# Kernel tuning notes

Measured on AMD Instinct MI355X. Metric: run time of the kernel, lower is better.

Reference implementation:

```python
import jax, jax.numpy as jnp
import numpy as np

N_NODES = 100000
N_EDGES = 1600000
N_FEAT = 32
HIDDEN = 96
N_GRAPHS = 2048


def setup_inputs() -> dict:
    key = jax.random.key(0)
    ks = jax.random.split(key, 16)
    x = jax.random.normal(ks[0], (N_NODES, N_FEAT), dtype=jnp.float32)
    edge_index = jax.random.randint(ks[1], (2, N_EDGES), 0, N_NODES, dtype=jnp.int64)
    batch = jnp.sort(jax.random.randint(ks[2], (N_NODES,), 0, N_GRAPHS, dtype=jnp.int64))

    def glorot(k, shape):
        lim = np.sqrt(6.0 / (shape[0] + shape[1]))
        return jax.random.uniform(k, shape, dtype=jnp.float32, minval=-lim, maxval=lim)

    return {
        "x": x, "edge_index": edge_index, "batch": batch,
        "W1": glorot(ks[3], (N_FEAT, HIDDEN)), "b1": jnp.zeros((HIDDEN,), jnp.float32),
        "W2": glorot(ks[4], (HIDDEN, HIDDEN)), "b2": jnp.zeros((HIDDEN,), jnp.float32),
        "W3": glorot(ks[5], (HIDDEN, HIDDEN)), "b3": jnp.zeros((HIDDEN,), jnp.float32),
        "W4": glorot(ks[6], (HIDDEN, HIDDEN)), "b4": jnp.zeros((HIDDEN,), jnp.float32),
        "Wf1": glorot(ks[7], (HIDDEN, 32)), "bf1": jnp.zeros((32,), jnp.float32),
        "Wf2": glorot(ks[8], (32, 1)), "bf2": jnp.zeros((1,), jnp.float32),
    }


def _gcn_norm(edge_index, num_nodes):
    # PyG GCNConv default: add self-loops, symmetric normalization D^-1/2 (A+I) D^-1/2
    loops = jnp.arange(num_nodes, dtype=edge_index.dtype)
    src = jnp.concatenate([edge_index[0], loops])
    dst = jnp.concatenate([edge_index[1], loops])
    deg = jax.ops.segment_sum(jnp.ones_like(dst, dtype=jnp.float32), dst, num_segments=num_nodes)
    dinv = jnp.where(deg > 0, jax.lax.rsqrt(jnp.where(deg > 0, deg, 1.0)), 0.0)
    norm = dinv[src] * dinv[dst]  # [E + N]
    return src, dst, norm


def _gcn_conv(x, src, dst, norm, W, b, num_nodes):
    xw = x @ W                      # [N, out]
    msg = xw[src] * norm[:, None]   # [E+N, out] gather + scale
    out = jax.ops.segment_sum(msg, dst, num_segments=num_nodes)  # scatter-add
    return out + b


def reference(x, edge_index, batch, W1, b1, W2, b2, W3, b3, W4, b4, Wf1, bf1, Wf2, bf2):
    n = x.shape[0]
    src, dst, norm = _gcn_norm(edge_index, n)
    h = jax.nn.relu(_gcn_conv(x, src, dst, norm, W1, b1, n))
    h = jax.nn.relu(_gcn_conv(h, src, dst, norm, W2, b2, n))
    h = jax.nn.relu(_gcn_conv(h, src, dst, norm, W3, b3, n))
    h = jax.nn.relu(_gcn_conv(h, src, dst, norm, W4, b4, n))
    g = jax.ops.segment_sum(h, batch, num_segments=N_GRAPHS)  # global_add_pool [G, 96]
    g = jax.nn.relu(g @ Wf1 + bf1)
    return g @ Wf2 + bf2  # [G, 1]
```

## Files before the change

kernel.cpp:

```cpp
#include <hip/hip_runtime.h>
#include <hip/hip_fp16.h>


#define HIDDEN 96

__device__ inline float4 h4_to_f4(uint2 u) {
    __half2 a = *reinterpret_cast<__half2*>(&u.x);
    __half2 b = *reinterpret_cast<__half2*>(&u.y);
    float2 fa = __half22float2(a), fb = __half22float2(b);
    return make_float4(fa.x, fa.y, fb.x, fb.y);
}

__device__ inline uint2 f4_to_h4(float4 v) {
    __half2 a = __float22half2_rn(make_float2(v.x, v.y));
    __half2 b = __float22half2_rn(make_float2(v.z, v.w));
    uint2 u;
    u.x = *reinterpret_cast<unsigned*>(&a);
    u.y = *reinterpret_cast<unsigned*>(&b);
    return u;
}

__global__ __launch_bounds__(256) void zero_int_kernel(int* p, int n) {
    int i = blockIdx.x * 256 + threadIdx.x;
    if (i < n) p[i] = 0;
}

__global__ __launch_bounds__(256) void zero_kernel(float* p, int n) {
    int i = blockIdx.x * 256 + threadIdx.x;
    if (i < n) p[i] = 0.0f;
}

__global__ __launch_bounds__(256) void cast_h_kernel(const float4* __restrict__ in,
                                                     uint2* __restrict__ out, int n4) {
    int i = blockIdx.x * 256 + threadIdx.x;
    if (i < n4) out[i] = f4_to_h4(in[i]);
}

__global__ __launch_bounds__(256) void deg_pos_kernel(const int* __restrict__ dst,
                                                      int* __restrict__ cnt,
                                                      int* __restrict__ epos, int E) {
    int e = blockIdx.x * 256 + threadIdx.x;
    if (e < E) epos[e] = atomicAdd(&cnt[dst[e]], 1);
}

__global__ __launch_bounds__(256) void dinv_kernel(const int* __restrict__ cnt,
                                                   float* __restrict__ dinv, int n) {
    int i = blockIdx.x * 256 + threadIdx.x;
    if (i < n) dinv[i] = rsqrtf((float)(cnt[i] + 1));
}

__global__ __launch_bounds__(256) void scan_reduce_kernel(const int* __restrict__ cnt,
                                                          int* __restrict__ bsum, int N) {
    __shared__ int s[256];
    int b = blockIdx.x, tid = threadIdx.x;
    int base = b * 1024;
    int v = 0;
    for (int j = tid; j < 1024; j += 256) {
        int i = base + j;
        v += (i < N) ? cnt[i] : 0;
    }
    s[tid] = v;
    __syncthreads();
    for (int off = 128; off > 0; off >>= 1) {
        if (tid < off) s[tid] += s[tid + off];
        __syncthreads();
    }
    if (tid == 0) bsum[b] = s[0];
}

__global__ __launch_bounds__(128) void scan_bsum_kernel(int* __restrict__ bsum, int nb) {
    __shared__ int s[128];
    int tid = threadIdx.x;
    int v = (tid < nb) ? bsum[tid] : 0;
    s[tid] = v;
    __syncthreads();
    for (int off = 1; off < 128; off <<= 1) {
        int t = (tid >= off) ? s[tid - off] : 0;
        __syncthreads();
        s[tid] += t;
        __syncthreads();
    }
    if (tid < nb) bsum[tid] = s[tid] - v;
}

__global__ __launch_bounds__(256) void scan_write_kernel(const int* __restrict__ cnt,
                                                         const int* __restrict__ bsum,
                                                         int* __restrict__ rowptr,
                                                         int N, int E) {
    __shared__ int ts[256];
    int b = blockIdx.x, tid = threadIdx.x;
    int base = b * 1024 + tid * 4;
    int v0 = (base + 0 < N) ? cnt[base + 0] : 0;
    int v1 = (base + 1 < N) ? cnt[base + 1] : 0;
    int v2 = (base + 2 < N) ? cnt[base + 2] : 0;
    int v3 = (base + 3 < N) ? cnt[base + 3] : 0;
    int sum = v0 + v1 + v2 + v3;
    ts[tid] = sum;
    __syncthreads();
    for (int off = 1; off < 256; off <<= 1) {
        int t = (tid >= off) ? ts[tid - off] : 0;
        __syncthreads();
        ts[tid] += t;
        __syncthreads();
    }
    int excl = bsum[b] + ts[tid] - sum;
    if (base + 0 < N) rowptr[base + 0] = excl;
    if (base + 1 < N) rowptr[base + 1] = excl + v0;
    if (base + 2 < N) rowptr[base + 2] = excl + v0 + v1;
    if (base + 3 < N) rowptr[base + 3] = excl + v0 + v1 + v2;
    if (b == 0 && tid == 0) rowptr[N] = E;
}

__global__ __launch_bounds__(256) void fill_csr_kernel(const int* __restrict__ src,
                                                       const int* __restrict__ dst,
                                                       const int* __restrict__ epos,
                                                       const float* __restrict__ dinv,
                                                       const int* __restrict__ rowptr,
                                                       int* __restrict__ col,
                                                       float* __restrict__ val, int E) {
    int e = blockIdx.x * 256 + threadIdx.x;
    if (e >= E) return;
    int s = src[e];
    int d = dst[e];
    int idx = rowptr[d] + epos[e];
    col[idx] = s;
    val[idx] = dinv[s] * dinv[d];
}

template <int K, bool RELU, bool BIAS, bool HALF_OUT>
__global__ __launch_bounds__(256) void gemm_kernel(const float* __restrict__ X,
                                                   const float* __restrict__ W,
                                                   const float* __restrict__ b,
                                                   void* __restrict__ Y, int n) {
    __shared__ float wlds[K * HIDDEN];
    for (int idx = threadIdx.x; idx < K * HIDDEN; idx += 256) wlds[idx] = W[idx];
    __syncthreads();

    int row = blockIdx.x * 256 + threadIdx.x;
    if (row >= n) return;

    float4 acc[24];
#pragma unroll
    for (int j = 0; j < 24; j++) acc[j] = make_float4(0.f, 0.f, 0.f, 0.f);

    const float4* wl4 = reinterpret_cast<const float4*>(wlds);
    const float4* xrow = reinterpret_cast<const float4*>(X + (size_t)row * K);

    for (int k0 = 0; k0 < K; k0 += 4) {
        float4 xv = xrow[k0 >> 2];
        if (RELU) {
            xv.x = fmaxf(xv.x, 0.f); xv.y = fmaxf(xv.y, 0.f);
            xv.z = fmaxf(xv.z, 0.f); xv.w = fmaxf(xv.w, 0.f);
        }
#pragma unroll
        for (int kk = 0; kk < 4; kk++) {
            float xs = (kk == 0) ? xv.x : (kk == 1) ? xv.y : (kk == 2) ? xv.z : xv.w;
#pragma unroll
            for (int j = 0; j < 24; j++) {
                float4 w = wl4[(k0 + kk) * 24 + j];
                acc[j].x += xs * w.x;
                acc[j].y += xs * w.y;
                acc[j].z += xs * w.z;
                acc[j].w += xs * w.w;
            }
        }
    }

#pragma unroll
    for (int j = 0; j < 24; j++) {
        if (BIAS) {
            float4 bb = reinterpret_cast<const float4*>(b)[j];
            acc[j].x += bb.x; acc[j].y += bb.y; acc[j].z += bb.z; acc[j].w += bb.w;
        }
    }
    if (HALF_OUT) {
        uint2* y2 = reinterpret_cast<uint2*>(Y) + (size_t)row * 24;
#pragma unroll
        for (int j = 0; j < 24; j++) y2[j] = f4_to_h4(acc[j]);
    } else {
        float4* y4 = reinterpret_cast<float4*>(Y) + (size_t)row * 24;
#pragma unroll
        for (int j = 0; j < 24; j++) y4[j] = acc[j];
    }
}

template <int TPN, bool POOL, bool BIAS>
__global__ __launch_bounds__(256) void aggregate_kernel(const uint2* __restrict__ xwh,
                                                        const int* __restrict__ rowptr,
                                                        const int* __restrict__ col,
                                                        const float* __restrict__ val,
                                                        const float* __restrict__ dinv,
                                                        const float* __restrict__ b,
                                                        float* __restrict__ out,
                                                        const int* __restrict__ batch,
                                                        float* __restrict__ gpool, int n) {
    unsigned t = blockIdx.x * 256 + threadIdx.x;
    unsigned i = t / (unsigned)TPN, q = t % (unsigned)TPN;
    if (i >= (unsigned)n) return;

    float dv = dinv[i];
    float s = dv * dv;
    float4 self = h4_to_f4(xwh[i * TPN + q]);
    float4 acc = make_float4(s * self.x, s * self.y, s * self.z, s * self.w);
    if (BIAS) {
        float4 bb = reinterpret_cast<const float4*>(b)[q];
        acc.x += bb.x; acc.y += bb.y; acc.z += bb.z; acc.w += bb.w;
    }

    int e = rowptr[i], end = rowptr[i + 1];
    for (; e + 3 < end; e += 4) {
        int c0 = col[e], c1 = col[e + 1], c2 = col[e + 2], c3 = col[e + 3];
        float w0 = val[e], w1 = val[e + 1], w2 = val[e + 2], w3 = val[e + 3];
        uint2 u0 = xwh[(unsigned)c0 * TPN + q];
        uint2 u1 = xwh[(unsigned)c1 * TPN + q];
        uint2 u2 = xwh[(unsigned)c2 * TPN + q];
        uint2 u3 = xwh[(unsigned)c3 * TPN + q];
        float4 v0 = h4_to_f4(u0), v1 = h4_to_f4(u1);
        float4 v2 = h4_to_f4(u2), v3 = h4_to_f4(u3);
        acc.x += w0 * v0.x + w1 * v1.x + w2 * v2.x + w3 * v3.x;
        acc.y += w0 * v0.y + w1 * v1.y + w2 * v2.y + w3 * v3.y;
        acc.z += w0 * v0.z + w1 * v1.z + w2 * v2.z + w3 * v3.z;
        acc.w += w0 * v0.w + w1 * v1.w + w2 * v2.w + w3 * v3.w;
    }
    for (; e < end; e++) {
        int c0 = col[e];
        float w0 = val[e];
        float4 g = h4_to_f4(xwh[(unsigned)c0 * TPN + q]);
        acc.x += w0 * g.x; acc.y += w0 * g.y;
        acc.z += w0 * g.z; acc.w += w0 * g.w;
    }

    if (POOL) {
        float* o = gpool + (size_t)batch[i] * (TPN * 4);
        unsigned fo = q * 4u;
        atomicAdd(o + fo + 0, fmaxf(acc.x, 0.f));
        atomicAdd(o + fo + 1, fmaxf(acc.y, 0.f));
        atomicAdd(o + fo + 2, fmaxf(acc.z, 0.f));
        atomicAdd(o + fo + 3, fmaxf(acc.w, 0.f));
    } else {
        reinterpret_cast<float4*>(out)[i * TPN + q] = acc;
    }
}

__global__ __launch_bounds__(64) void mlp_kernel(const float* __restrict__ g,
                                                 const float* __restrict__ Wf1,
                                                 const float* __restrict__ bf1,
                                                 const float* __restrict__ Wf2,
                                                 const float* __restrict__ bf2,
                                                 float* __restrict__ out, int G) {
    __shared__ float gs[HIDDEN];
    __shared__ float hid[32];
    int blk = blockIdx.x;
    int lane = threadIdx.x;
    for (int idx = lane; idx < HIDDEN; idx += 64) gs[idx] = g[(size_t)blk * HIDDEN + idx];
    __syncthreads();
    if (lane < 32) {
        float a = bf1[lane];
        for (int k = 0; k < HIDDEN; k++) a = fmaf(gs[k], Wf1[k * 32 + lane], a);
        hid[lane] = fmaxf(a, 0.f);
    }
    __syncthreads();
    if (lane == 0) {
        float o = bf2[0];
        for (int k = 0; k < 32; k++) o = fmaf(hid[k], Wf2[k], o);
        out[blk] = o;
    }
}

extern "C" void kernel_launch(void* const* d_in, const int* in_sizes, int n_in,
                              void* d_out, int out_size, void* d_ws, size_t ws_size,
                              hipStream_t stream) {
    const float* x     = (const float*)d_in[0];
    const int*   ei    = (const int*)d_in[1];
    const int*   batch = (const int*)d_in[2];
    const float* W1 = (const float*)d_in[3];  const float* b1 = (const float*)d_in[4];
    const float* W2 = (const float*)d_in[5];  const float* b2 = (const float*)d_in[6];
    const float* W3 = (const float*)d_in[7];  const float* b3 = (const float*)d_in[8];
    const float* W4 = (const float*)d_in[9];  const float* b4 = (const float*)d_in[10];
    const float* Wf1 = (const float*)d_in[11]; const float* bf1 = (const float*)d_in[12];
    const float* Wf2 = (const float*)d_in[13]; const float* bf2 = (const float*)d_in[14];
    float* out = (float*)d_out;

    int N = in_sizes[0] / 32;
    int E = in_sizes[1] / 2;
    int G = out_size;
    const int* src = ei;
    const int* dst = ei + E;

    char* ws = (char*)d_ws;
    size_t off = 0;
    auto alloc = [&](size_t bytes) -> void* {
        void* p = (void*)(ws + off);
        off += (bytes + 255) & ~(size_t)255;
        return p;
    };
    int*   degcnt = (int*)alloc((size_t)N * 4);
    float* dinv   = (float*)alloc((size_t)N * 4);
    int*   rowptr = (int*)alloc((size_t)(N + 1) * 4);
    int*   bsum   = (int*)alloc((size_t)128 * 4);
    int*   col    = (int*)alloc((size_t)E * 4);
    float* val    = (float*)alloc((size_t)E * 4);
    float* bufA   = (float*)alloc((size_t)N * 32 * 4);
    float* bufB   = (float*)alloc((size_t)N * HIDDEN * 4);
    uint2* bufH   = (uint2*)alloc((size_t)N * HIDDEN * 2);
    uint2* xh     = (uint2*)alloc((size_t)N * 32 * 2);
    float* gbuf   = (float*)alloc((size_t)G * HIDDEN * 4);
    (void)ws_size;

    int* epos = (int*)bufA;
    float* aggX = bufA;

    int gN   = (N + 255) / 256;
    int gE   = (E + 255) / 256;
    int gAgg32 = (int)(((long long)N * 8 + 255) / 256);
    int gAgg96 = (int)(((long long)N * 24 + 255) / 256);
    int nb   = (N + 1023) / 1024;

    zero_int_kernel<<<gN, 256, 0, stream>>>(degcnt, N);
    deg_pos_kernel<<<gE, 256, 0, stream>>>(dst, degcnt, epos, E);
    dinv_kernel<<<gN, 256, 0, stream>>>(degcnt, dinv, N);
    scan_reduce_kernel<<<nb, 256, 0, stream>>>(degcnt, bsum, N);
    scan_bsum_kernel<<<1, 128, 0, stream>>>(bsum, nb);
    scan_write_kernel<<<nb, 256, 0, stream>>>(degcnt, bsum, rowptr, N, E);
    fill_csr_kernel<<<gE, 256, 0, stream>>>(src, dst, epos, dinv, rowptr, col, val, E);

    cast_h_kernel<<<(N * 8 + 255) / 256, 256, 0, stream>>>(
        reinterpret_cast<const float4*>(x), xh, N * 8);
    aggregate_kernel<8, false, false><<<gAgg32, 256, 0, stream>>>(
        xh, rowptr, col, val, dinv, nullptr, aggX, nullptr, nullptr, N);
    gemm_kernel<32, false, true, false><<<gN, 256, 0, stream>>>(aggX, W1, b1, bufB, N);

    gemm_kernel<96, true, false, true><<<gN, 256, 0, stream>>>(bufB, W2, nullptr, bufH, N);
    aggregate_kernel<24, false, true><<<gAgg96, 256, 0, stream>>>(
        bufH, rowptr, col, val, dinv, b2, bufB, nullptr, nullptr, N);

    gemm_kernel<96, true, false, true><<<gN, 256, 0, stream>>>(bufB, W3, nullptr, bufH, N);
    aggregate_kernel<24, false, true><<<gAgg96, 256, 0, stream>>>(
        bufH, rowptr, col, val, dinv, b3, bufB, nullptr, nullptr, N);

    zero_kernel<<<(G * HIDDEN + 255) / 256, 256, 0, stream>>>(gbuf, G * HIDDEN);
    gemm_kernel<96, true, false, true><<<gN, 256, 0, stream>>>(bufB, W4, nullptr, bufH, N);
    aggregate_kernel<24, true, true><<<gAgg96, 256, 0, stream>>>(
        bufH, rowptr, col, val, dinv, b4, nullptr, batch, gbuf, N);

    mlp_kernel<<<G, 64, 0, stream>>>(gbuf, Wf1, bf1, Wf2, bf2, out, G);
}
```

Before: 704.8 us.

## Pad CSR rows to multiples of eight and store intermediates in fp16

Each CSR row is padded to a multiple of 8 entries, with zero col and val in the padding, so the aggregation loop issues vectorized int4/float4 loads of col and val and 8 gathers per iteration with no remainder loop. All intermediate activations (aggregation outputs and first GEMM output) are now stored in half precision, which halves the traffic of the GEMM and aggregate intermediates. In exchange there is extra zeroing of the padded col/val arrays, wasted gathers of row 0 for padding slots, and lower precision in the intermediate activations.

```diff
diff --git a/kernel.cpp b/kernel.cpp
--- a/kernel.cpp
+++ b/kernel.cpp
@@ -19,6 +19,8 @@
     u.y = *reinterpret_cast<unsigned*>(&b);
     return u;
 }
+
+__device__ inline int pad8(int c) { return (c + 7) & ~7; }
 
 __global__ __launch_bounds__(256) void zero_int_kernel(int* p, int n) {
     int i = blockIdx.x * 256 + threadIdx.x;
@@ -57,7 +59,7 @@
     int v = 0;
     for (int j = tid; j < 1024; j += 256) {
         int i = base + j;
-        v += (i < N) ? cnt[i] : 0;
+        v += (i < N) ? pad8(cnt[i]) : 0;
     }
     s[tid] = v;
     __syncthreads();
@@ -85,15 +87,14 @@
 
 __global__ __launch_bounds__(256) void scan_write_kernel(const int* __restrict__ cnt,
                                                          const int* __restrict__ bsum,
-                                                         int* __restrict__ rowptr,
-                                                         int N, int E) {
+                                                         int* __restrict__ rowptr, int N) {
     __shared__ int ts[256];
     int b = blockIdx.x, tid = threadIdx.x;
     int base = b * 1024 + tid * 4;
-    int v0 = (base + 0 < N) ? cnt[base + 0] : 0;
-    int v1 = (base + 1 < N) ? cnt[base + 1] : 0;
-    int v2 = (base + 2 < N) ? cnt[base + 2] : 0;
-    int v3 = (base + 3 < N) ? cnt[base + 3] : 0;
+    int v0 = (base + 0 < N) ? pad8(cnt[base + 0]) : 0;
+    int v1 = (base + 1 < N) ? pad8(cnt[base + 1]) : 0;
+    int v2 = (base + 2 < N) ? pad8(cnt[base + 2]) : 0;
+    int v3 = (base + 3 < N) ? pad8(cnt[base + 3]) : 0;
     int sum = v0 + v1 + v2 + v3;
     ts[tid] = sum;
     __syncthreads();
@@ -104,11 +105,10 @@
         __syncthreads();
     }
     int excl = bsum[b] + ts[tid] - sum;
-    if (base + 0 < N) rowptr[base + 0] = excl;
-    if (base + 1 < N) rowptr[base + 1] = excl + v0;
-    if (base + 2 < N) rowptr[base + 2] = excl + v0 + v1;
-    if (base + 3 < N) rowptr[base + 3] = excl + v0 + v1 + v2;
-    if (b == 0 && tid == 0) rowptr[N] = E;
+    if (base + 0 <= N) rowptr[base + 0] = excl;
+    if (base + 1 <= N) rowptr[base + 1] = excl + v0;
+    if (base + 2 <= N) rowptr[base + 2] = excl + v0 + v1;
+    if (base + 3 <= N) rowptr[base + 3] = excl + v0 + v1 + v2;
 }
 
 __global__ __launch_bounds__(256) void fill_csr_kernel(const int* __restrict__ src,
@@ -127,11 +127,11 @@
     val[idx] = dinv[s] * dinv[d];
 }
 
-template <int K, bool RELU, bool BIAS, bool HALF_OUT>
-__global__ __launch_bounds__(256) void gemm_kernel(const float* __restrict__ X,
+template <int K, bool RELU, bool BIAS>
+__global__ __launch_bounds__(256) void gemm_kernel(const uint2* __restrict__ X,
                                                    const float* __restrict__ W,
                                                    const float* __restrict__ b,
-                                                   void* __restrict__ Y, int n) {
+                                                   uint2* __restrict__ Y, int n) {
     __shared__ float wlds[K * HIDDEN];
     for (int idx = threadIdx.x; idx < K * HIDDEN; idx += 256) wlds[idx] = W[idx];
     __syncthreads();
@@ -144,10 +144,10 @@
     for (int j = 0; j < 24; j++) acc[j] = make_float4(0.f, 0.f, 0.f, 0.f);
 
     const float4* wl4 = reinterpret_cast<const float4*>(wlds);
-    const float4* xrow = reinterpret_cast<const float4*>(X + (size_t)row * K);
+    const uint2* xrow = X + (size_t)row * (K / 4);
 
     for (int k0 = 0; k0 < K; k0 += 4) {
-        float4 xv = xrow[k0 >> 2];
+        float4 xv = h4_to_f4(xrow[k0 >> 2]);
         if (RELU) {
             xv.x = fmaxf(xv.x, 0.f); xv.y = fmaxf(xv.y, 0.f);
             xv.z = fmaxf(xv.z, 0.f); xv.w = fmaxf(xv.w, 0.f);
@@ -166,21 +166,14 @@
         }
     }
 
+    uint2* y2 = Y + (size_t)row * 24;
 #pragma unroll
     for (int j = 0; j < 24; j++) {
         if (BIAS) {
             float4 bb = reinterpret_cast<const float4*>(b)[j];
             acc[j].x += bb.x; acc[j].y += bb.y; acc[j].z += bb.z; acc[j].w += bb.w;
         }
-    }
-    if (HALF_OUT) {
-        uint2* y2 = reinterpret_cast<uint2*>(Y) + (size_t)row * 24;
-#pragma unroll
-        for (int j = 0; j < 24; j++) y2[j] = f4_to_h4(acc[j]);
-    } else {
-        float4* y4 = reinterpret_cast<float4*>(Y) + (size_t)row * 24;
-#pragma unroll
-        for (int j = 0; j < 24; j++) y4[j] = acc[j];
+        y2[j] = f4_to_h4(acc[j]);
     }
 }
 
@@ -191,7 +184,7 @@
                                                         const float* __restrict__ val,
                                                         const float* __restrict__ dinv,
                                                         const float* __restrict__ b,
-                                                        float* __restrict__ out,
+                                                        uint2* __restrict__ out,
                                                         const int* __restrict__ batch,
                                                         float* __restrict__ gpool, int n) {
     unsigned t = blockIdx.x * 256 + threadIdx.x;
@@ -208,26 +201,31 @@
     }
 
     int e = rowptr[i], end = rowptr[i + 1];
-    for (; e + 3 < end; e += 4) {
-        int c0 = col[e], c1 = col[e + 1], c2 = col[e + 2], c3 = col[e + 3];
-        float w0 = val[e], w1 = val[e + 1], w2 = val[e + 2], w3 = val[e + 3];
-        uint2 u0 = xwh[(unsigned)c0 * TPN + q];
-        uint2 u1 = xwh[(unsigned)c1 * TPN + q];
-        uint2 u2 = xwh[(unsigned)c2 * TPN + q];
-        uint2 u3 = xwh[(unsigned)c3 * TPN + q];
+    for (; e < end; e += 8) {
+        int4 ca = *reinterpret_cast<const int4*>(col + e);
+        int4 cb = *reinterpret_cast<const int4*>(col + e + 4);
+        float4 wa = *reinterpret_cast<const float4*>(val + e);
+        float4 wb = *reinterpret_cast<const float4*>(val + e + 4);
+        uint2 u0 = xwh[(unsigned)ca.x * TPN + q];
+        uint2 u1 = xwh[(unsigned)ca.y * TPN + q];
+        uint2 u2 = xwh[(unsigned)ca.z * TPN + q];
+        uint2 u3 = xwh[(unsigned)ca.w * TPN + q];
+        uint2 u4 = xwh[(unsigned)cb.x * TPN + q];
+        uint2 u5 = xwh[(unsigned)cb.y * TPN + q];
+        uint2 u6 = xwh[(unsigned)cb.z * TPN + q];
+        uint2 u7 = xwh[(unsigned)cb.w * TPN + q];
         float4 v0 = h4_to_f4(u0), v1 = h4_to_f4(u1);
         float4 v2 = h4_to_f4(u2), v3 = h4_to_f4(u3);
-        acc.x += w0 * v0.x + w1 * v1.x + w2 * v2.x + w3 * v3.x;
-        acc.y += w0 * v0.y + w1 * v1.y + w2 * v2.y + w3 * v3.y;
-        acc.z += w0 * v0.z + w1 * v1.z + w2 * v2.z + w3 * v3.z;
-        acc.w += w0 * v0.w + w1 * v1.w + w2 * v2.w + w3 * v3.w;
-    }
-    for (; e < end; e++) {
-        int c0 = col[e];
-        float w0 = val[e];
-        float4 g = h4_to_f4(xwh[(unsigned)c0 * TPN + q]);
-        acc.x += w0 * g.x; acc.y += w0 * g.y;
-        acc.z += w0 * g.z; acc.w += w0 * g.w;
+        float4 v4 = h4_to_f4(u4), v5 = h4_to_f4(u5);
+        float4 v6 = h4_to_f4(u6), v7 = h4_to_f4(u7);
+        acc.x += wa.x * v0.x + wa.y * v1.x + wa.z * v2.x + wa.w * v3.x
+               + wb.x * v4.x + wb.y * v5.x + wb.z * v6.x + wb.w * v7.x;
+        acc.y += wa.x * v0.y + wa.y * v1.y + wa.z * v2.y + wa.w * v3.y
+               + wb.x * v4.y + wb.y * v5.y + wb.z * v6.y + wb.w * v7.y;
+        acc.z += wa.x * v0.z + wa.y * v1.z + wa.z * v2.z + wa.w * v3.z
+               + wb.x * v4.z + wb.y * v5.z + wb.z * v6.z + wb.w * v7.z;
+        acc.w += wa.x * v0.w + wa.y * v1.w + wa.z * v2.w + wa.w * v3.w
+               + wb.x * v4.w + wb.y * v5.w + wb.z * v6.w + wb.w * v7.w;
     }
 
     if (POOL) {
@@ -238,7 +236,7 @@
         atomicAdd(o + fo + 2, fmaxf(acc.z, 0.f));
         atomicAdd(o + fo + 3, fmaxf(acc.w, 0.f));
     } else {
-        reinterpret_cast<float4*>(out)[i * TPN + q] = acc;
+        out[i * TPN + q] = f4_to_h4(acc);
     }
 }
 
@@ -286,6 +284,7 @@
     int G = out_size;
     const int* src = ei;
     const int* dst = ei + E;
+    int Emax = E + 8 * N;
 
     char* ws = (char*)d_ws;
     size_t off = 0;
@@ -298,48 +297,49 @@
     float* dinv   = (float*)alloc((size_t)N * 4);
     int*   rowptr = (int*)alloc((size_t)(N + 1) * 4);
     int*   bsum   = (int*)alloc((size_t)128 * 4);
-    int*   col    = (int*)alloc((size_t)E * 4);
-    float* val    = (float*)alloc((size_t)E * 4);
-    float* bufA   = (float*)alloc((size_t)N * 32 * 4);
-    float* bufB   = (float*)alloc((size_t)N * HIDDEN * 4);
+    int*   col    = (int*)alloc((size_t)Emax * 4);
+    float* val    = (float*)alloc((size_t)Emax * 4);
+    int*   epos   = (int*)alloc((size_t)E * 4);
+    uint2* xh     = (uint2*)alloc((size_t)N * 32 * 2);
+    uint2* aggXh  = (uint2*)alloc((size_t)N * 32 * 2);
+    uint2* bufB   = (uint2*)alloc((size_t)N * HIDDEN * 2);
     uint2* bufH   = (uint2*)alloc((size_t)N * HIDDEN * 2);
-    uint2* xh     = (uint2*)alloc((size_t)N * 32 * 2);
     float* gbuf   = (float*)alloc((size_t)G * HIDDEN * 4);
     (void)ws_size;
 
-    int* epos = (int*)bufA;
-    float* aggX = bufA;
-
     int gN   = (N + 255) / 256;
     int gE   = (E + 255) / 256;
+    int gEm  = (Emax + 255) / 256;
     int gAgg32 = (int)(((long long)N * 8 + 255) / 256);
     int gAgg96 = (int)(((long long)N * 24 + 255) / 256);
     int nb   = (N + 1023) / 1024;
 
     zero_int_kernel<<<gN, 256, 0, stream>>>(degcnt, N);
+    zero_int_kernel<<<gEm, 256, 0, stream>>>(col, Emax);
+    zero_kernel<<<gEm, 256, 0, stream>>>(val, Emax);
     deg_pos_kernel<<<gE, 256, 0, stream>>>(dst, degcnt, epos, E);
     dinv_kernel<<<gN, 256, 0, stream>>>(degcnt, dinv, N);
     scan_reduce_kernel<<<nb, 256, 0, stream>>>(degcnt, bsum, N);
     scan_bsum_kernel<<<1, 128, 0, stream>>>(bsum, nb);
-    scan_write_kernel<<<nb, 256, 0, stream>>>(degcnt, bsum, rowptr, N, E);
+    scan_write_kernel<<<nb, 256, 0, stream>>>(degcnt, bsum, rowptr, N);
     fill_csr_kernel<<<gE, 256, 0, stream>>>(src, dst, epos, dinv, rowptr, col, val, E);
 
     cast_h_kernel<<<(N * 8 + 255) / 256, 256, 0, stream>>>(
         reinterpret_cast<const float4*>(x), xh, N * 8);
     aggregate_kernel<8, false, false><<<gAgg32, 256, 0, stream>>>(
-        xh, rowptr, col, val, dinv, nullptr, aggX, nullptr, nullptr, N);
-    gemm_kernel<32, false, true, false><<<gN, 256, 0, stream>>>(aggX, W1, b1, bufB, N);
-
-    gemm_kernel<96, true, false, true><<<gN, 256, 0, stream>>>(bufB, W2, nullptr, bufH, N);
+        xh, rowptr, col, val, dinv, nullptr, aggXh, nullptr, nullptr, N);
+    gemm_kernel<32, false, true><<<gN, 256, 0, stream>>>(aggXh, W1, b1, bufB, N);
+
+    gemm_kernel<96, true, false><<<gN, 256, 0, stream>>>(bufB, W2, nullptr, bufH, N);
     aggregate_kernel<24, false, true><<<gAgg96, 256, 0, stream>>>(
         bufH, rowptr, col, val, dinv, b2, bufB, nullptr, nullptr, N);
 
-    gemm_kernel<96, true, false, true><<<gN, 256, 0, stream>>>(bufB, W3, nullptr, bufH, N);
+    gemm_kernel<96, true, false><<<gN, 256, 0, stream>>>(bufB, W3, nullptr, bufH, N);
     aggregate_kernel<24, false, true><<<gAgg96, 256, 0, stream>>>(
         bufH, rowptr, col, val, dinv, b3, bufB, nullptr, nullptr, N);
 
     zero_kernel<<<(G * HIDDEN + 255) / 256, 256, 0, stream>>>(gbuf, G * HIDDEN);
-    gemm_kernel<96, true, false, true><<<gN, 256, 0, stream>>>(bufB, W4, nullptr, bufH, N);
+    gemm_kernel<96, true, false><<<gN, 256, 0, stream>>>(bufB, W4, nullptr, bufH, N);
     aggregate_kernel<24, true, true><<<gAgg96, 256, 0, stream>>>(
         bufH, rowptr, col, val, dinv, b4, nullptr, batch, gbuf, N);
 
```

New measurement: 696.5 us. Within noise of the previous version (-1.2%).
